# Performance work log

Measured on AMD Instinct MI355X. Metric: run time of the kernel, lower is better.

## Reference

```python
import jax, jax.numpy as jnp
from jax import lax
import numpy as np

LSTM = 128      # encoder hidden per direction
H2 = 2 * LSTM   # decoder hidden / bi-encoder output dim
E = 1024        # embedding dim
V = 30611       # vocab
A = 64          # attention dim
B, S, T = 16, 400, 96
START_TOK = 101


def setup_inputs() -> dict:
    key = jax.random.key(0)
    ks = jax.random.split(key, 24)
    d = {}
    d["word_embedding"] = jax.random.normal(ks[0], (V, E), jnp.float32) * 0.05
    d["article"] = jax.random.randint(ks[1], (B, S), 0, V)
    d["article_length"] = jax.random.randint(ks[2], (B,), S // 2, S + 1)
    d["abstract"] = jax.random.randint(ks[3], (B, T), 0, V)

    def p(k, shape, scale):
        return jax.random.normal(k, shape, jnp.float32) * scale

    # encoder BiLSTM (PyTorch gate order i,f,g,o), forward and backward dirs
    d["enc_Wih_f"] = p(ks[4], (4 * LSTM, E), 0.03)
    d["enc_Whh_f"] = p(ks[5], (4 * LSTM, LSTM), 0.08)
    d["enc_b_f"] = jnp.zeros((4 * LSTM,), jnp.float32)
    d["enc_Wih_b"] = p(ks[6], (4 * LSTM, E), 0.03)
    d["enc_Whh_b"] = p(ks[7], (4 * LSTM, LSTM), 0.08)
    d["enc_b_b"] = jnp.zeros((4 * LSTM,), jnp.float32)
    # decoder LSTM: input = embed(1024) + context(256)
    d["dec_Wih"] = p(ks[8], (4 * H2, E + H2), 0.03)
    d["dec_Whh"] = p(ks[9], (4 * H2, H2), 0.06)
    d["dec_b"] = jnp.zeros((4 * H2,), jnp.float32)
    # vocab prediction
    d["pred_W"] = p(ks[10], (V, H2), 0.06)
    d["pred_b"] = jnp.zeros((V,), jnp.float32)
    # additive attention
    d["attn_s_W"] = p(ks[11], (A, H2), 0.06)
    d["attn_s_b"] = jnp.zeros((A,), jnp.float32)
    d["attn_h_W"] = p(ks[12], (A, H2), 0.06)
    d["attn_h_b"] = jnp.zeros((A,), jnp.float32)
    d["attn_f_W"] = p(ks[13], (1, A), 0.12)
    d["attn_f_b"] = jnp.zeros((1,), jnp.float32)
    return d


def _lstm_cell(x, h, c, Wih, Whh, b):
    g = x @ Wih.T + h @ Whh.T + b
    i, f, gg, o = jnp.split(g, 4, axis=-1)
    c = jax.nn.sigmoid(f) * c + jax.nn.sigmoid(i) * jnp.tanh(gg)
    h = jax.nn.sigmoid(o) * jnp.tanh(c)
    return h, c


def reference(word_embedding, article, article_length, abstract,
              enc_Wih_f, enc_Whh_f, enc_b_f, enc_Wih_b, enc_Whh_b, enc_b_b,
              dec_Wih, dec_Whh, dec_b, pred_W, pred_b,
              attn_s_W, attn_s_b, attn_h_W, attn_h_b, attn_f_W, attn_f_b):
    dt = word_embedding.dtype
    # ---- encoder ----
    xe = word_embedding[article]          # [B,S,E]
    xs = xe.transpose(1, 0, 2)            # [S,B,E]
    z = jnp.zeros((B, LSTM), dt)

    def fstep(carry, x):
        h, c = carry
        h, c = _lstm_cell(x, h, c, enc_Wih_f, enc_Whh_f, enc_b_f)
        return (h, c), h

    def bstep(carry, x):
        h, c = carry
        h, c = _lstm_cell(x, h, c, enc_Wih_b, enc_Whh_b, enc_b_b)
        return (h, c), h

    (hf, cf_f), out_f = lax.scan(fstep, (z, z), xs)
    (hb, cf_b), out_b = lax.scan(bstep, (z, z), xs, reverse=True)
    enc_out = jnp.concatenate([out_f, out_b], axis=-1).transpose(1, 0, 2)  # [B,S,2H]

    # decoder init state = concat of final fwd/bwd encoder states
    h0 = jnp.concatenate([hf, hb], axis=-1)   # [B,H2]
    c0 = jnp.concatenate([cf_f, cf_b], axis=-1)

    # attention mask: (+9999 valid, -9999 pad); min(score, mask) keeps valid scores
    length = jnp.clip(article_length, 1, S)
    pos = jnp.arange(S)
    mask = jnp.where(pos[None, :] < length[:, None], 9999.0, -9999.0).astype(dt)

    enc_ws = enc_out @ attn_s_W.T + attn_s_b  # [B,S,A], precomputed per original code

    # teacher forcing inputs: step 0 uses token 101, step t uses abstract[:, t-1]
    tokens_in = jnp.concatenate(
        [jnp.full((B, 1), START_TOK, dtype=abstract.dtype), abstract[:, :-1]], axis=1)
    emb_in = word_embedding[tokens_in].transpose(1, 0, 2)  # [T,B,E]

    def dstep(carry, emb):
        h, c, ctx = carry
        x = jnp.concatenate([emb, ctx], axis=-1)           # [B,E+H2]
        h, c = _lstm_cell(x, h, c, dec_Wih, dec_Whh, dec_b)
        logits = h @ pred_W.T + pred_b                     # [B,V]
        wh = h @ attn_h_W.T + attn_h_b                     # [B,A]
        score = jnp.tanh(enc_ws + wh[:, None, :]) @ attn_f_W[0] + attn_f_b[0]  # [B,S]
        score = jnp.minimum(score, mask)
        w = jax.nn.softmax(score, axis=-1)
        ctx = jnp.einsum('bs,bsd->bd', w, enc_out)         # [B,H2]
        return (h, c, ctx), logits

    ctx0 = jnp.zeros((B, H2), dt)
    _, logits = lax.scan(dstep, (h0, c0, ctx0), emb_in)    # [T,B,V]

    logits = logits.transpose(1, 0, 2).reshape(B * T, V)
    tgt = abstract.reshape(-1)
    logp = jax.nn.log_softmax(logits, axis=-1)
    nll = -jnp.take_along_axis(logp, tgt[:, None], axis=1)[:, 0]
    valid = (tgt != 0).astype(logits.dtype)                # ignore_index=0
    loss = jnp.sum(nll * valid) / jnp.maximum(jnp.sum(valid), 1.0)
    return loss
```

## Files before the change

kernel.cpp:

```cpp
#include <hip/hip_runtime.h>
#include <cmath>

#define NB 16
#define SS 400
#define TT 96
#define HL 128
#define HH 256
#define AA 64
#define VV 30611
#define VVP 30720
#define START_TOK 101
#define NCHUNK 120

typedef __attribute__((ext_vector_type(8))) short bf16x8;
typedef __attribute__((ext_vector_type(4))) float f32x4;

#define PIN4(v) asm volatile("" : "+v"((v).x), "+v"((v).y), "+v"((v).z), "+v"((v).w))
#define LBAR() asm volatile("s_waitcnt lgkmcnt(0)\n\ts_barrier" ::: "memory")

__device__ __forceinline__ float gload(const float* p) {
  return __hip_atomic_load(p, __ATOMIC_RELAXED, __HIP_MEMORY_SCOPE_AGENT);
}
__device__ __forceinline__ void gstore(float* p, float v) {
  __hip_atomic_store(p, v, __ATOMIC_RELAXED, __HIP_MEMORY_SCOPE_AGENT);
}
__device__ __forceinline__ float sigmf(float x) { return 1.0f / (1.0f + __expf(-x)); }
__device__ __forceinline__ float tanhf_(float x) {
  float xc = fminf(fmaxf(x, -15.0f), 15.0f);
  return 1.0f - 2.0f / (__expf(2.0f * xc) + 1.0f);
}
__device__ __forceinline__ short f2bf(float f) {
  unsigned u = __float_as_uint(f);
  unsigned r = (u + 0x7FFFu + ((u >> 16) & 1u)) >> 16;
  return (short)r;
}
__device__ __forceinline__ void flagbar(int* flags, int b, int g, int target) {
  __syncthreads();
  if (threadIdx.x == 0)
    __hip_atomic_store(&flags[b*8 + g], target, __ATOMIC_RELAXED, __HIP_MEMORY_SCOPE_AGENT);
  if (threadIdx.x < 8) {
    while (__hip_atomic_load(&flags[b*8 + threadIdx.x], __ATOMIC_RELAXED, __HIP_MEMORY_SCOPE_AGENT) < target)
      __builtin_amdgcn_s_sleep(1);
  }
  LBAR();
}

__global__ __launch_bounds__(256) void k_init(int* flags) {
  if (threadIdx.x < 128) flags[threadIdx.x] = 0;
}

__global__ __launch_bounds__(256) void k_casts(
    const float* __restrict__ wf, const float* __restrict__ wb,
    const float* __restrict__ dwih,
    short* __restrict__ wfB, short* __restrict__ wbB, short* __restrict__ dwB)
{
  const int stride = gridDim.x * 256;
  const int t0 = blockIdx.x * 256 + threadIdx.x;
  for (int i = t0; i < 512*1024; i += stride) wfB[i] = f2bf(wf[i]);
  for (int i = t0; i < 512*1024; i += stride) wbB[i] = f2bf(wb[i]);
  for (int i = t0; i < 1024*1024; i += stride) {
    int r = i >> 10, k = i & 1023;
    dwB[i] = f2bf(dwih[r*1280 + k]);
  }
}

__global__ __launch_bounds__(256) void k_embproj_enc_mfma(
    const float* __restrict__ emb, const int* __restrict__ article,
    const short* __restrict__ wfB, const short* __restrict__ wbB,
    const float* __restrict__ bf, const float* __restrict__ bb,
    float* __restrict__ xcomb)
{
  const int m0 = blockIdx.x * 64;
  const int n0 = blockIdx.y * 256;
  const int t = threadIdx.x;
  const int w = t >> 6, l = t & 63;
  __shared__ short Abuf[64*136];
  __shared__ int tok[64];
  if (t < 64) {
    int R = m0 + t, s = R >> 4, b = R & 15;
    tok[t] = article[b*SS + s];
  }
  const short* __restrict__ Wb = (n0 < 512) ? wfB : wbB;
  const int nb0 = (n0 < 512) ? n0 : (n0 - 512);
  f32x4 acc[4][4];
  #pragma unroll
  for (int i = 0; i < 4; ++i)
    #pragma unroll
    for (int j = 0; j < 4; ++j) acc[i][j] = (f32x4){0.f,0.f,0.f,0.f};
  __syncthreads();
  const int ar = t >> 2, ak0 = (t & 3) * 32;
  for (int kc = 0; kc < 8; ++kc) {
    const float* src = emb + (size_t)tok[ar]*1024 + kc*128 + ak0;
    #pragma unroll
    for (int j = 0; j < 8; ++j) {
      float4 v = *(const float4*)(src + 4*j);
      short4 s4; s4.x = f2bf(v.x); s4.y = f2bf(v.y); s4.z = f2bf(v.z); s4.w = f2bf(v.w);
      *(short4*)(&Abuf[ar*136 + ak0 + 4*j]) = s4;
    }
    LBAR();
    #pragma unroll
    for (int ks = 0; ks < 4; ++ks) {
      bf16x8 af[4];
      #pragma unroll
      for (int mr = 0; mr < 4; ++mr)
        af[mr] = *(const bf16x8*)(&Abuf[(mr*16 + (l & 15))*136 + ks*32 + (l >> 4)*8]);
      #pragma unroll
      for (int ct = 0; ct < 4; ++ct) {
        int n = nb0 + w*64 + ct*16 + (l & 15);
        bf16x8 bfr = *(const bf16x8*)(Wb + (size_t)n*1024 + kc*128 + ks*32 + (l >> 4)*8);
        #pragma unroll
        for (int mr = 0; mr < 4; ++mr)
          acc[mr][ct] = __builtin_amdgcn_mfma_f32_16x16x32_bf16(af[mr], bfr, acc[mr][ct], 0, 0, 0);
      }
    }
    LBAR();
  }
  #pragma unroll
  for (int ct = 0; ct < 4; ++ct) {
    int n = n0 + w*64 + ct*16 + (l & 15);
    float bias = (n < 512) ? bf[n] : bb[n - 512];
    #pragma unroll
    for (int mr = 0; mr < 4; ++mr) {
      #pragma unroll
      for (int r = 0; r < 4; ++r) {
        int R = m0 + mr*16 + (l >> 4)*4 + r;
        xcomb[(size_t)R*1024 + n] = acc[mr][ct][r] + bias;
      }
    }
  }
}

__global__ __launch_bounds__(1024, 4) void k_encoder(
    const float* __restrict__ xcomb,
    const float* __restrict__ whhf, const float* __restrict__ whhb,
    float* __restrict__ encout,
    float* __restrict__ hpub,
    float* __restrict__ c0buf,
    const float* __restrict__ predW, short* __restrict__ predWb,
    const float* __restrict__ emb, const int* __restrict__ abstr,
    const short* __restrict__ dwB, const float* __restrict__ db,
    float* __restrict__ decpre)
{
  const int t = threadIdx.x;
  __shared__ float hl[128];
  __shared__ float part[2][512];
  __shared__ short Abuf[64*136];
  __shared__ int tok[64];

  if (blockIdx.x >= 56) {
    const size_t idx0 = (size_t)(blockIdx.x - 56) * 1024 + t;
    const size_t stride = (size_t)200 * 1024;
    for (size_t i = idx0; i < (size_t)VVP*256; i += stride)
      predWb[i] = (i < (size_t)VV*256) ? f2bf(predW[i]) : (short)0;
    return;
  }
  if (blockIdx.x >= 32) {
    const int m0 = (blockIdx.x - 32) * 64;
    const int sub = t & 255, w2 = t >> 8;
    const int w = sub >> 6, l = sub & 63;
    if (t < 64) {
      int R = m0 + t, tt2 = R >> 4, bb = R & 15;
      tok[t] = (tt2 == 0) ? START_TOK : abstr[bb*TT + tt2 - 1];
    }
    f32x4 acc[4][4];
    #pragma unroll
    for (int i = 0; i < 4; ++i)
      #pragma unroll
      for (int j = 0; j < 4; ++j) acc[i][j] = (f32x4){0.f,0.f,0.f,0.f};
    __syncthreads();
    const int ar = sub >> 2, ak0 = (sub & 3) * 32;
    for (int kc = 0; kc < 8; ++kc) {
      if (w2 == 0) {
        const float* src = emb + (size_t)tok[ar]*1024 + kc*128 + ak0;
        #pragma unroll
        for (int j = 0; j < 8; ++j) {
          float4 v = *(const float4*)(src + 4*j);
          short4 s4; s4.x = f2bf(v.x); s4.y = f2bf(v.y); s4.z = f2bf(v.z); s4.w = f2bf(v.w);
          *(short4*)(&Abuf[ar*136 + ak0 + 4*j]) = s4;
        }
      }
      LBAR();
      #pragma unroll
      for (int ks = 0; ks < 4; ++ks) {
        bf16x8 af[4];
        #pragma unroll
        for (int mr = 0; mr < 4; ++mr)
          af[mr] = *(const bf16x8*)(&Abuf[(mr*16 + (l & 15))*136 + ks*32 + (l >> 4)*8]);
        #pragma unroll
        for (int ct = 0; ct < 4; ++ct) {
          int n = w2*256 + w*64 + ct*16 + (l & 15);
          bf16x8 bfr = *(const bf16x8*)(dwB + (size_t)n*1024 + kc*128 + ks*32 + (l >> 4)*8);
          #pragma unroll
          for (int mr = 0; mr < 4; ++mr)
            acc[mr][ct] = __builtin_amdgcn_mfma_f32_16x16x32_bf16(af[mr], bfr, acc[mr][ct], 0, 0, 0);
        }
      }
      LBAR();
    }
    #pragma unroll
    for (int ct = 0; ct < 4; ++ct) {
      int n = w2*256 + w*64 + ct*16 + (l & 15);
      float bias = db[n];
      #pragma unroll
      for (int mr = 0; mr < 4; ++mr) {
        #pragma unroll
        for (int r = 0; r < 4; ++r) {
          int R = m0 + mr*16 + (l >> 4)*4 + r;
          decpre[(size_t)R*1024 + n] = acc[mr][ct][r] + bias;
        }
      }
    }
    return;
  }
  const int b = blockIdx.x & 15, dir = blockIdx.x >> 4;
  const int row = t & 511;
  const int ks = t >> 9;
  const float* __restrict__ Whh = dir ? whhb : whhf;
  float4 wr[16];
  #pragma unroll
  for (int j = 0; j < 16; ++j) {
    wr[j] = *(const float4*)(Whh + row*128 + ks*64 + j*4);
    PIN4(wr[j]);
  }
  float c_reg = 0.0f;
  if (t < 128) hl[t] = 0.0f;
  float xv0 = 0.f, xv1 = 0.f, xv2 = 0.f, xv3 = 0.f;
  if (t < 128) {
    const float* xr = xcomb + ((dir ? (SS-1) : 0)*NB + b)*1024 + dir*512 + t;
    xv0 = xr[0]; xv1 = xr[128]; xv2 = xr[256]; xv3 = xr[384];
  }
  __syncthreads();
  for (int s = 0; s < SS; ++s) {
    const int sf = dir ? (SS-1-s) : s;
    const float* hs = hl + ks*64;
    float a0 = 0.f, a1 = 0.f, a2 = 0.f, a3 = 0.f;
    #pragma unroll
    for (int j = 0; j < 16; j += 4) {
      float4 h0 = *(const float4*)(hs + j*4);
      float4 h1 = *(const float4*)(hs + j*4 + 4);
      float4 h2 = *(const float4*)(hs + j*4 + 8);
      float4 h3 = *(const float4*)(hs + j*4 + 12);
      a0 += wr[j].x*h0.x + wr[j].y*h0.y + wr[j].z*h0.z + wr[j].w*h0.w;
      a1 += wr[j+1].x*h1.x + wr[j+1].y*h1.y + wr[j+1].z*h1.z + wr[j+1].w*h1.w;
      a2 += wr[j+2].x*h2.x + wr[j+2].y*h2.y + wr[j+2].z*h2.z + wr[j+2].w*h2.w;
      a3 += wr[j+3].x*h3.x + wr[j+3].y*h3.y + wr[j+3].z*h3.z + wr[j+3].w*h3.w;
    }
    part[ks][row] = (a0 + a1) + (a2 + a3);
    float nx0 = 0.f, nx1 = 0.f, nx2 = 0.f, nx3 = 0.f;
    if (t < 128 && s + 1 < SS) {
      const int sfn = dir ? (SS-2-s) : (s+1);
      const float* xr = xcomb + (sfn*NB + b)*1024 + dir*512 + t;
      nx0 = xr[0]; nx1 = xr[128]; nx2 = xr[256]; nx3 = xr[384];
    }
    LBAR();
    if (t < 128) {
      float gi = part[0][t]       + part[1][t]       + xv0;
      float gf = part[0][128 + t] + part[1][128 + t] + xv1;
      float gg = part[0][256 + t] + part[1][256 + t] + xv2;
      float go = part[0][384 + t] + part[1][384 + t] + xv3;
      float iv = sigmf(gi), fv = sigmf(gf), gv = tanhf_(gg), ov = sigmf(go);
      c_reg = fv*c_reg + iv*gv;
      float hv = ov*tanhf_(c_reg);
      hl[t] = hv;
      encout[(b*SS + sf)*HH + dir*HL + t] = hv;
    }
    LBAR();
    xv0 = nx0; xv1 = nx1; xv2 = nx2; xv3 = nx3;
  }
  if (t < 128) {
    hpub[b*HH + dir*HL + t] = hl[t];
    c0buf[b*HH + dir*HL + t] = c_reg;
  }
}

__global__ __launch_bounds__(256) void k_encws(
    const float* __restrict__ encout,
    const float* __restrict__ asW, const float* __restrict__ asb,
    float* __restrict__ encwsR)
{
  const int rt = blockIdx.x;
  const int tid = threadIdx.x;
  __shared__ float Al[32*260];
  #pragma unroll
  for (int i = 0; i < 32; ++i) {
    int l = tid + i*256;
    int r = l >> 8, k = l & 255;
    Al[r*260 + k] = encout[(rt*32 + r)*256 + k];
  }
  __syncthreads();
  const int a = tid & 63, rg = tid >> 6;
  float acc[8];
  #pragma unroll
  for (int q = 0; q < 8; ++q) acc[q] = 0.0f;
  const float4* w4 = (const float4*)(asW + a*256);
  for (int k4 = 0; k4 < 64; ++k4) {
    float4 w = w4[k4];
    #pragma unroll
    for (int q = 0; q < 8; ++q) {
      const float4* a4 = (const float4*)(Al + (rg*8 + q)*260);
      float4 av = a4[k4];
      acc[q] += av.x*w.x + av.y*w.y + av.z*w.z + av.w*w.w;
    }
  }
  float bias = asb[a];
  #pragma unroll
  for (int q = 0; q < 8; ++q) {
    int row = rt*32 + rg*8 + q;
    encwsR[row*64 + a] = acc[q] + bias;
  }
}

__global__ __launch_bounds__(1024, 4) void k_decoder(
    const float* __restrict__ decpre,
    const float* __restrict__ dwhh,
    const float* __restrict__ dwih,
    const float* __restrict__ ahW, const float* __restrict__ ahb,
    const float* __restrict__ afW, const float* __restrict__ afb,
    const float* __restrict__ encwsR,
    const float* __restrict__ encout,
    const int* __restrict__ alen,
    const float* __restrict__ c0buf,
    float* hpub, float* cpub, float* wpub,
    float* __restrict__ dhall,
    int* flags)
{
  const int wg = blockIdx.x;
  const int g = wg >> 4, b = wg & 15;
  const int t = threadIdx.x;
  const int r = t & 127, ks = t >> 7;
  const int lane = t & 63;
  const int u = t & 31;
  const int s0 = g*50;

  const int grow = (r >> 5)*256 + g*32 + (r & 31);
  float4 wr[16];
  #pragma unroll
  for (int j = 0; j < 16; ++j) {
    int k = ks*64 + j*4;
    wr[j] = (k < 256) ? *(const float4*)(dwhh + grow*256 + k)
                      : *(const float4*)(dwih + grow*1280 + 1024 + (k - 256));
    PIN4(wr[j]);
  }

  __shared__ float encl[50*256];
  __shared__ float wsl[50*68];
  __shared__ float ahWt[32*68];
  __shared__ float hc[512];
  __shared__ float part[8][132];
  __shared__ float wh[64];
  __shared__ float fwl[64];
  __shared__ float scl[64];
  __shared__ float sh_m, sh_s;

  for (int i = t; i < 50*256; i += 1024) {
    int si = i >> 8, d = i & 255;
    encl[i] = encout[(b*SS + s0 + si)*HH + d];
  }
  for (int i = t; i < 50*64; i += 1024) {
    int si = i >> 6, a = i & 63;
    wsl[si*68 + a] = encwsR[(b*SS + s0 + si)*64 + a];
  }
  for (int i = t; i < 32*64; i += 1024) {
    int u2 = i >> 6, a = i & 63;
    ahWt[u2*68 + a] = ahW[a*HH + g*32 + u2];
  }
  if (t < 64) fwl[t] = afW[t];
  const float fb0 = afb[0];
  int len = alen[b]; len = min(max(len, 1), SS);
  float c_reg = 0.f;
  float pre0 = 0.f, pre1 = 0.f, pre2 = 0.f, pre3 = 0.f;
  if (t < 256) {
    c_reg = c0buf[b*HH + g*32 + u];
    hc[t] = gload(hpub + b*HH + t);
    hc[256 + t] = 0.0f;
    const float* pr = decpre + (size_t)(0*NB + b)*1024 + g*32 + u;
    pre0 = pr[0]; pre1 = pr[256]; pre2 = pr[512]; pre3 = pr[768];
  }
  __syncthreads();

  for (int tt = 0; tt < TT; ++tt) {
    {
      const float* hs = hc + ks*64;
      float a0 = 0.f, a1 = 0.f, a2 = 0.f, a3 = 0.f;
      #pragma unroll
      for (int j = 0; j < 16; j += 4) {
        float4 h0 = *(const float4*)(hs + j*4);
        float4 h1 = *(const float4*)(hs + j*4 + 4);
        float4 h2 = *(const float4*)(hs + j*4 + 8);
        float4 h3 = *(const float4*)(hs + j*4 + 12);
        a0 += wr[j].x*h0.x + wr[j].y*h0.y + wr[j].z*h0.z + wr[j].w*h0.w;
        a1 += wr[j+1].x*h1.x + wr[j+1].y*h1.y + wr[j+1].z*h1.z + wr[j+1].w*h1.w;
        a2 += wr[j+2].x*h2.x + wr[j+2].y*h2.y + wr[j+2].z*h2.z + wr[j+2].w*h2.w;
        a3 += wr[j+3].x*h3.x + wr[j+3].y*h3.y + wr[j+3].z*h3.z + wr[j+3].w*h3.w;
      }
      part[ks][r] = (a0 + a1) + (a2 + a3);
    }
    LBAR();
    if (t < 256) {
      float g0 = pre0, g1 = pre1, g2 = pre2, g3 = pre3;
      #pragma unroll
      for (int j = 0; j < 8; ++j) {
        g0 += part[j][u];
        g1 += part[j][32 + u];
        g2 += part[j][64 + u];
        g3 += part[j][96 + u];
      }
      float iv = sigmf(g0), fv = sigmf(g1), gv = tanhf_(g2), ov = sigmf(g3);
      c_reg = fv*c_reg + iv*gv;
      float hv = ov*tanhf_(c_reg);
      if (t < 32) {
        gstore(hpub + b*HH + g*32 + t, hv);
        dhall[(tt*NB + b)*HH + g*32 + t] = hv;
      }
      int wv = t >> 6;
      int a = wv*16 + (lane >> 2);
      int j4 = lane & 3;
      float wacc = 0.f;
      #pragma unroll
      for (int i = 0; i < 8; ++i) {
        int u2 = j4*8 + i;
        float hx = __shfl(hv, u2, 64);
        wacc += ahWt[u2*68 + a] * hx;
      }
      wacc += __shfl_xor(wacc, 1);
      wacc += __shfl_xor(wacc, 2);
      if (j4 == 0) gstore(wpub + (b*8 + g)*72 + a, wacc);
    }
    flagbar(flags, b, g, 2*tt + 1);
    if (t < 256) {
      hc[t] = gload(hpub + b*HH + t);
      if (tt + 1 < TT) {
        const float* pr = decpre + (size_t)((tt+1)*NB + b)*1024 + g*32 + u;
        pre0 = pr[0]; pre1 = pr[256]; pre2 = pr[512]; pre3 = pr[768];
      }
    } else if (t < 320) {
      int a = t - 256;
      float s = ahb[a];
      #pragma unroll
      for (int j = 0; j < 8; ++j) s += gload(wpub + (b*8 + j)*72 + a);
      wh[a] = s;
    }
    LBAR();
    if (t < 800) {
      int s = t >> 4, j = t & 15;
      const float* wrow = wsl + s*68 + j*4;
      float p = fwl[j*4]   * tanhf_(wrow[0] + wh[j*4])
              + fwl[j*4+1] * tanhf_(wrow[1] + wh[j*4+1])
              + fwl[j*4+2] * tanhf_(wrow[2] + wh[j*4+2])
              + fwl[j*4+3] * tanhf_(wrow[3] + wh[j*4+3]);
      p += __shfl_xor(p, 1);
      p += __shfl_xor(p, 2);
      p += __shfl_xor(p, 4);
      p += __shfl_xor(p, 8);
      if (j == 0) scl[s] = p;
    }
    LBAR();
    if (t < 64) {
      float sc = -1e30f;
      if (t < 50) {
        sc = fb0 + scl[t];
        sc = fminf(sc, (s0 + t < len) ? 9999.0f : -9999.0f);
      }
      float m = sc;
      #pragma unroll
      for (int o = 32; o; o >>= 1) m = fmaxf(m, __shfl_xor(m, o));
      float p = (t < 50) ? __expf(sc - m) : 0.0f;
      scl[t] = p;
      float ssum = p;
      #pragma unroll
      for (int o = 32; o; o >>= 1) ssum += __shfl_xor(ssum, o);
      if (t == 0) { sh_m = m; sh_s = ssum; }
    }
    LBAR();
    if (t < 256) {
      float acc = 0.0f;
      const float* eb = encl + t;
      #pragma unroll 10
      for (int i = 0; i < 50; ++i) acc += scl[i] * eb[i*256];
      gstore(cpub + (b*8 + g)*272 + t, acc);
      if (t == 0) gstore(cpub + (b*8 + g)*272 + 256, sh_m);
      if (t == 1) gstore(cpub + (b*8 + g)*272 + 257, sh_s);
    }
    flagbar(flags, b, g, 2*tt + 2);
    if (t < 256) {
      float mj[8], sj[8];
      #pragma unroll
      for (int j = 0; j < 8; ++j) {
        mj[j] = gload(cpub + (b*8 + j)*272 + 256);
        sj[j] = gload(cpub + (b*8 + j)*272 + 257);
      }
      float M = mj[0];
      #pragma unroll
      for (int j = 1; j < 8; ++j) M = fmaxf(M, mj[j]);
      float denom = 0.f, ctx = 0.f;
      #pragma unroll
      for (int j = 0; j < 8; ++j) {
        float e = __expf(mj[j] - M);
        denom += sj[j] * e;
        ctx += gload(cpub + (b*8 + j)*272 + t) * e;
      }
      hc[256 + t] = ctx / denom;
    }
    LBAR();
  }
}

__global__ __launch_bounds__(256) void k_pred_mfma(
    const float* __restrict__ dhall,
    const short* __restrict__ predWb,
    const float* __restrict__ predb,
    float* __restrict__ pm, float* __restrict__ ps)
{
  const int m0 = blockIdx.x * 64;
  const int ch = blockIdx.y;
  const int c0 = ch * 256;
  const int t = threadIdx.x;
  const int w = t >> 6, l = t & 63;
  __shared__ __align__(16) char smem[64*264*4];
  short* Abuf = (short*)smem;
  float* L    = (float*)smem;
  __shared__ float red[256];
  __shared__ float rowmax[64];

  {
    const int ar = t >> 2, ak0 = (t & 3) * 64;
    const float* src = dhall + (size_t)(m0 + ar)*256 + ak0;
    #pragma unroll
    for (int j = 0; j < 16; ++j) {
      float4 v = *(const float4*)(src + 4*j);
      short4 s4; s4.x = f2bf(v.x); s4.y = f2bf(v.y); s4.z = f2bf(v.z); s4.w = f2bf(v.w);
      *(short4*)(&Abuf[ar*264 + ak0 + 4*j]) = s4;
    }
  }
  LBAR();
  f32x4 acc[4][4];
  #pragma unroll
  for (int i = 0; i < 4; ++i)
    #pragma unroll
    for (int j = 0; j < 4; ++j) acc[i][j] = (f32x4){0.f,0.f,0.f,0.f};
  #pragma unroll
  for (int kst = 0; kst < 8; ++kst) {
    bf16x8 af[4];
    #pragma unroll
    for (int mr = 0; mr < 4; ++mr)
      af[mr] = *(const bf16x8*)(&Abuf[(mr*16 + (l & 15))*264 + kst*32 + (l >> 4)*8]);
    #pragma unroll
    for (int ct = 0; ct < 4; ++ct) {
      int col = c0 + w*64 + ct*16 + (l & 15);
      bf16x8 bfr = *(const bf16x8*)(predWb + (size_t)col*256 + kst*32 + (l >> 4)*8);
      #pragma unroll
      for (int mr = 0; mr < 4; ++mr)
        acc[mr][ct] = __builtin_amdgcn_mfma_f32_16x16x32_bf16(af[mr], bfr, acc[mr][ct], 0, 0, 0);
    }
  }
  LBAR();
  #pragma unroll
  for (int ct = 0; ct < 4; ++ct) {
    int col = c0 + w*64 + ct*16 + (l & 15);
    float bias = (col < VV) ? predb[col] : 0.0f;
    bool valid = (col < VV);
    #pragma unroll
    for (int mr = 0; mr < 4; ++mr) {
      #pragma unroll
      for (int r = 0; r < 4; ++r) {
        int rl = mr*16 + (l >> 4)*4 + r;
        L[rl*264 + w*64 + ct*16 + (l & 15)] = valid ? (acc[mr][ct][r] + bias) : -1e30f;
      }
    }
  }
  LBAR();
  {
    const int row = t & 63, qd = t >> 6;
    float m = -1e30f;
    const float* Lr = L + row*264 + qd*64;
    for (int i = 0; i < 64; ++i) m = fmaxf(m, Lr[i]);
    red[qd*64 + row] = m;
  }
  LBAR();
  if (t < 64) {
    float m = fmaxf(fmaxf(red[t], red[64+t]), fmaxf(red[128+t], red[192+t]));
    rowmax[t] = m;
  }
  LBAR();
  {
    const int row = t & 63, qd = t >> 6;
    float m = rowmax[row];
    float ssum = 0.f;
    const float* Lr = L + row*264 + qd*64;
    for (int i = 0; i < 64; ++i) ssum += __expf(Lr[i] - m);
    red[qd*64 + row] = ssum;
  }
  LBAR();
  if (t < 64) {
    float ssum = red[t] + red[64+t] + red[128+t] + red[192+t];
    pm[(m0 + t)*NCHUNK + ch] = rowmax[t];
    ps[(m0 + t)*NCHUNK + ch] = ssum;
  }
}

__global__ __launch_bounds__(256) void k_loss_part(
    const float* __restrict__ pm, const float* __restrict__ ps,
    const float* __restrict__ dhall,
    const float* __restrict__ predW, const float* __restrict__ predb,
    const int* __restrict__ abstr, float* __restrict__ lpart)
{
  const int tid = threadIdx.x;
  const int row = blockIdx.x*256 + tid;
  __shared__ float rs[256], rc[256];
  float lsum = 0.0f, lcnt = 0.0f;
  {
    int t = row >> 4, b = row & 15;
    int tok = abstr[b*TT + t];
    float m = -1e30f;
    for (int c = 0; c < NCHUNK; ++c) m = fmaxf(m, pm[row*NCHUNK + c]);
    float ss = 0.0f;
    for (int c = 0; c < NCHUNK; ++c) ss += ps[row*NCHUNK + c] * __expf(pm[row*NCHUNK + c] - m);
    float lse = m + __logf(ss);
    float tl = predb[tok];
    const float* hrow = dhall + row*256;
    const float* wrow = predW + tok*256;
    #pragma unroll 4
    for (int k = 0; k < 256; ++k) tl += hrow[k] * wrow[k];
    if (tok != 0) { lsum = lse - tl; lcnt = 1.0f; }
  }
  rs[tid] = lsum; rc[tid] = lcnt;
  __syncthreads();
  for (int st = 128; st; st >>= 1) {
    if (tid < st) { rs[tid] += rs[tid + st]; rc[tid] += rc[tid + st]; }
    __syncthreads();
  }
  if (tid == 0) { lpart[blockIdx.x*2] = rs[0]; lpart[blockIdx.x*2 + 1] = rc[0]; }
}

__global__ void k_loss_final(const float* __restrict__ lpart, float* __restrict__ out) {
  if (threadIdx.x == 0) {
    float s = 0.f, c = 0.f;
    for (int i = 0; i < 6; ++i) { s += lpart[i*2]; c += lpart[i*2 + 1]; }
    out[0] = s / fmaxf(c, 1.0f);
  }
}

extern "C" void kernel_launch(void* const* d_in, const int* in_sizes, int n_in,
                              void* d_out, int out_size, void* d_ws, size_t ws_size,
                              hipStream_t stream) {
  const float* emb   = (const float*)d_in[0];
  const int* article = (const int*)d_in[1];
  const int* alen    = (const int*)d_in[2];
  const int* abstr   = (const int*)d_in[3];
  const float* eWihF = (const float*)d_in[4];
  const float* eWhhF = (const float*)d_in[5];
  const float* ebF   = (const float*)d_in[6];
  const float* eWihB = (const float*)d_in[7];
  const float* eWhhB = (const float*)d_in[8];
  const float* ebB   = (const float*)d_in[9];
  const float* dWih  = (const float*)d_in[10];
  const float* dWhh  = (const float*)d_in[11];
  const float* db    = (const float*)d_in[12];
  const float* pW    = (const float*)d_in[13];
  const float* pb    = (const float*)d_in[14];
  const float* asW   = (const float*)d_in[15];
  const float* asb   = (const float*)d_in[16];
  const float* ahW   = (const float*)d_in[17];
  const float* ahb   = (const float*)d_in[18];
  const float* afW   = (const float*)d_in[19];
  const float* afb   = (const float*)d_in[20];
  float* out = (float*)d_out;

  float* w = (float*)d_ws;
  size_t o = 0;
  float* xcomb  = w + o; o += (size_t)SS*NB*1024;
  float* encout = w + o; o += (size_t)NB*SS*HH;
  float* encwsR = w + o; o += (size_t)NB*SS*AA;
  float* decpre = w + o; o += (size_t)TT*NB*1024;
  float* dhall  = w + o; o += (size_t)TT*NB*HH;
  float* hpub   = w + o; o += NB*HH;
  float* cpub   = w + o; o += NB*8*272;
  float* wpub   = w + o; o += NB*8*72;
  float* c0buf  = w + o; o += NB*HH;
  float* pm     = w + o; o += (size_t)TT*NB*NCHUNK;
  float* ps     = w + o; o += (size_t)TT*NB*NCHUNK;
  float* lpart  = w + o; o += 16;
  int* flags = (int*)(w + o); o += 128;
  short* predWb = (short*)(w + o); o += (size_t)VVP*256/2;
  short* wfB    = (short*)(w + o); o += 512*1024/2;
  short* wbB    = (short*)(w + o); o += 512*1024/2;
  short* dwB    = (short*)(w + o); o += 1024*1024/2;

  k_init<<<1, 256, 0, stream>>>(flags);
  k_casts<<<512, 256, 0, stream>>>(eWihF, eWihB, dWih, wfB, wbB, dwB);
  k_embproj_enc_mfma<<<dim3(100, 4), 256, 0, stream>>>(emb, article, wfB, wbB, ebF, ebB, xcomb);
  k_encoder<<<256, 1024, 0, stream>>>(xcomb, eWhhF, eWhhB, encout, hpub, c0buf,
                                      pW, predWb, emb, abstr, dwB, db, decpre);
  k_encws<<<200, 256, 0, stream>>>(encout, asW, asb, encwsR);
  k_decoder<<<128, 1024, 0, stream>>>(decpre, dWhh, dWih, ahW, ahb, afW, afb,
                                      encwsR, encout, alen, c0buf, hpub, cpub, wpub, dhall, flags);
  k_pred_mfma<<<dim3(24, 120), 256, 0, stream>>>(dhall, predWb, pb, pm, ps);
  k_loss_part<<<6, 256, 0, stream>>>(pm, ps, dhall, pW, pb, abstr, lpart);
  k_loss_final<<<1, 64, 0, stream>>>(lpart, out);
}
```

Before: 1.604 ms.

## Fuse decoder and vocab projection into one persistent kernel with progress flags

Merges the decoder recurrence, the encoder attention projection (previously a separate k_encws kernel) and the vocab-prediction GEMM into one launch of 256 workgroups. The first 128 workgroups run the recurrent decoder and publish per-batch progress counters. The other 128 poll those counters and compute logits plus per-chunk softmax statistics for completed timestep groups while decoding continues. This overlaps the large vocab GEMM with the latency-bound serial decoder and removes two launches. The risks are that the spin-waiting workgroups must be co-resident with the decoder workgroups to avoid deadlock, and that the prediction workgroups now use 1024 threads with smaller per-wave tiles.

After: 1.809 ms. +12.8%, slower.

```diff
diff --git a/kernel.cpp b/kernel.cpp
--- a/kernel.cpp
+++ b/kernel.cpp
@@ -21,6 +21,9 @@
 __device__ __forceinline__ float gload(const float* p) {
   return __hip_atomic_load(p, __ATOMIC_RELAXED, __HIP_MEMORY_SCOPE_AGENT);
 }
+__device__ __forceinline__ int gload_i(const int* p) {
+  return __hip_atomic_load(p, __ATOMIC_RELAXED, __HIP_MEMORY_SCOPE_AGENT);
+}
 __device__ __forceinline__ void gstore(float* p, float v) {
   __hip_atomic_store(p, v, __ATOMIC_RELAXED, __HIP_MEMORY_SCOPE_AGENT);
 }
@@ -46,7 +49,7 @@
 }
 
 __global__ __launch_bounds__(256) void k_init(int* flags) {
-  if (threadIdx.x < 128) flags[threadIdx.x] = 0;
+  if (threadIdx.x < 160) flags[threadIdx.x] = 0;
 }
 
 __global__ __launch_bounds__(256) void k_casts(
@@ -273,328 +276,306 @@
   }
 }
 
-__global__ __launch_bounds__(256) void k_encws(
-    const float* __restrict__ encout,
-    const float* __restrict__ asW, const float* __restrict__ asb,
-    float* __restrict__ encwsR)
-{
-  const int rt = blockIdx.x;
-  const int tid = threadIdx.x;
-  __shared__ float Al[32*260];
-  #pragma unroll
-  for (int i = 0; i < 32; ++i) {
-    int l = tid + i*256;
-    int r = l >> 8, k = l & 255;
-    Al[r*260 + k] = encout[(rt*32 + r)*256 + k];
-  }
-  __syncthreads();
-  const int a = tid & 63, rg = tid >> 6;
-  float acc[8];
-  #pragma unroll
-  for (int q = 0; q < 8; ++q) acc[q] = 0.0f;
-  const float4* w4 = (const float4*)(asW + a*256);
-  for (int k4 = 0; k4 < 64; ++k4) {
-    float4 w = w4[k4];
-    #pragma unroll
-    for (int q = 0; q < 8; ++q) {
-      const float4* a4 = (const float4*)(Al + (rg*8 + q)*260);
-      float4 av = a4[k4];
-      acc[q] += av.x*w.x + av.y*w.y + av.z*w.z + av.w*w.w;
-    }
-  }
-  float bias = asb[a];
-  #pragma unroll
-  for (int q = 0; q < 8; ++q) {
-    int row = rt*32 + rg*8 + q;
-    encwsR[row*64 + a] = acc[q] + bias;
-  }
-}
-
-__global__ __launch_bounds__(1024, 4) void k_decoder(
+__global__ __launch_bounds__(1024, 4) void k_decoder_pred(
     const float* __restrict__ decpre,
     const float* __restrict__ dwhh,
     const float* __restrict__ dwih,
     const float* __restrict__ ahW, const float* __restrict__ ahb,
     const float* __restrict__ afW, const float* __restrict__ afb,
-    const float* __restrict__ encwsR,
+    const float* __restrict__ asW, const float* __restrict__ asb,
     const float* __restrict__ encout,
     const int* __restrict__ alen,
     const float* __restrict__ c0buf,
     float* hpub, float* cpub, float* wpub,
     float* __restrict__ dhall,
-    int* flags)
-{
-  const int wg = blockIdx.x;
-  const int g = wg >> 4, b = wg & 15;
-  const int t = threadIdx.x;
-  const int r = t & 127, ks = t >> 7;
-  const int lane = t & 63;
-  const int u = t & 31;
-  const int s0 = g*50;
-
-  const int grow = (r >> 5)*256 + g*32 + (r & 31);
-  float4 wr[16];
-  #pragma unroll
-  for (int j = 0; j < 16; ++j) {
-    int k = ks*64 + j*4;
-    wr[j] = (k < 256) ? *(const float4*)(dwhh + grow*256 + k)
-                      : *(const float4*)(dwih + grow*1280 + 1024 + (k - 256));
-    PIN4(wr[j]);
-  }
-
-  __shared__ float encl[50*256];
-  __shared__ float wsl[50*68];
-  __shared__ float ahWt[32*68];
-  __shared__ float hc[512];
-  __shared__ float part[8][132];
-  __shared__ float wh[64];
-  __shared__ float fwl[64];
-  __shared__ float scl[64];
-  __shared__ float sh_m, sh_s;
-
-  for (int i = t; i < 50*256; i += 1024) {
-    int si = i >> 8, d = i & 255;
-    encl[i] = encout[(b*SS + s0 + si)*HH + d];
-  }
-  for (int i = t; i < 50*64; i += 1024) {
-    int si = i >> 6, a = i & 63;
-    wsl[si*68 + a] = encwsR[(b*SS + s0 + si)*64 + a];
-  }
-  for (int i = t; i < 32*64; i += 1024) {
-    int u2 = i >> 6, a = i & 63;
-    ahWt[u2*68 + a] = ahW[a*HH + g*32 + u2];
-  }
-  if (t < 64) fwl[t] = afW[t];
-  const float fb0 = afb[0];
-  int len = alen[b]; len = min(max(len, 1), SS);
-  float c_reg = 0.f;
-  float pre0 = 0.f, pre1 = 0.f, pre2 = 0.f, pre3 = 0.f;
-  if (t < 256) {
-    c_reg = c0buf[b*HH + g*32 + u];
-    hc[t] = gload(hpub + b*HH + t);
-    hc[256 + t] = 0.0f;
-    const float* pr = decpre + (size_t)(0*NB + b)*1024 + g*32 + u;
-    pre0 = pr[0]; pre1 = pr[256]; pre2 = pr[512]; pre3 = pr[768];
-  }
-  __syncthreads();
-
-  for (int tt = 0; tt < TT; ++tt) {
-    {
-      const float* hs = hc + ks*64;
-      float a0 = 0.f, a1 = 0.f, a2 = 0.f, a3 = 0.f;
-      #pragma unroll
-      for (int j = 0; j < 16; j += 4) {
-        float4 h0 = *(const float4*)(hs + j*4);
-        float4 h1 = *(const float4*)(hs + j*4 + 4);
-        float4 h2 = *(const float4*)(hs + j*4 + 8);
-        float4 h3 = *(const float4*)(hs + j*4 + 12);
-        a0 += wr[j].x*h0.x + wr[j].y*h0.y + wr[j].z*h0.z + wr[j].w*h0.w;
-        a1 += wr[j+1].x*h1.x + wr[j+1].y*h1.y + wr[j+1].z*h1.z + wr[j+1].w*h1.w;
-        a2 += wr[j+2].x*h2.x + wr[j+2].y*h2.y + wr[j+2].z*h2.z + wr[j+2].w*h2.w;
-        a3 += wr[j+3].x*h3.x + wr[j+3].y*h3.y + wr[j+3].z*h3.z + wr[j+3].w*h3.w;
-      }
-      part[ks][r] = (a0 + a1) + (a2 + a3);
-    }
-    LBAR();
-    if (t < 256) {
-      float g0 = pre0, g1 = pre1, g2 = pre2, g3 = pre3;
-      #pragma unroll
-      for (int j = 0; j < 8; ++j) {
-        g0 += part[j][u];
-        g1 += part[j][32 + u];
-        g2 += part[j][64 + u];
-        g3 += part[j][96 + u];
-      }
-      float iv = sigmf(g0), fv = sigmf(g1), gv = tanhf_(g2), ov = sigmf(g3);
-      c_reg = fv*c_reg + iv*gv;
-      float hv = ov*tanhf_(c_reg);
-      if (t < 32) {
-        gstore(hpub + b*HH + g*32 + t, hv);
-        dhall[(tt*NB + b)*HH + g*32 + t] = hv;
-      }
-      int wv = t >> 6;
-      int a = wv*16 + (lane >> 2);
-      int j4 = lane & 3;
-      float wacc = 0.f;
-      #pragma unroll
-      for (int i = 0; i < 8; ++i) {
-        int u2 = j4*8 + i;
-        float hx = __shfl(hv, u2, 64);
-        wacc += ahWt[u2*68 + a] * hx;
-      }
-      wacc += __shfl_xor(wacc, 1);
-      wacc += __shfl_xor(wacc, 2);
-      if (j4 == 0) gstore(wpub + (b*8 + g)*72 + a, wacc);
-    }
-    flagbar(flags, b, g, 2*tt + 1);
-    if (t < 256) {
-      hc[t] = gload(hpub + b*HH + t);
-      if (tt + 1 < TT) {
-        const float* pr = decpre + (size_t)((tt+1)*NB + b)*1024 + g*32 + u;
-        pre0 = pr[0]; pre1 = pr[256]; pre2 = pr[512]; pre3 = pr[768];
-      }
-    } else if (t < 320) {
-      int a = t - 256;
-      float s = ahb[a];
-      #pragma unroll
-      for (int j = 0; j < 8; ++j) s += gload(wpub + (b*8 + j)*72 + a);
-      wh[a] = s;
-    }
-    LBAR();
-    if (t < 800) {
-      int s = t >> 4, j = t & 15;
-      const float* wrow = wsl + s*68 + j*4;
-      float p = fwl[j*4]   * tanhf_(wrow[0] + wh[j*4])
-              + fwl[j*4+1] * tanhf_(wrow[1] + wh[j*4+1])
-              + fwl[j*4+2] * tanhf_(wrow[2] + wh[j*4+2])
-              + fwl[j*4+3] * tanhf_(wrow[3] + wh[j*4+3]);
-      p += __shfl_xor(p, 1);
-      p += __shfl_xor(p, 2);
-      p += __shfl_xor(p, 4);
-      p += __shfl_xor(p, 8);
-      if (j == 0) scl[s] = p;
-    }
-    LBAR();
-    if (t < 64) {
-      float sc = -1e30f;
-      if (t < 50) {
-        sc = fb0 + scl[t];
-        sc = fminf(sc, (s0 + t < len) ? 9999.0f : -9999.0f);
-      }
-      float m = sc;
-      #pragma unroll
-      for (int o = 32; o; o >>= 1) m = fmaxf(m, __shfl_xor(m, o));
-      float p = (t < 50) ? __expf(sc - m) : 0.0f;
-      scl[t] = p;
-      float ssum = p;
-      #pragma unroll
-      for (int o = 32; o; o >>= 1) ssum += __shfl_xor(ssum, o);
-      if (t == 0) { sh_m = m; sh_s = ssum; }
-    }
-    LBAR();
-    if (t < 256) {
-      float acc = 0.0f;
-      const float* eb = encl + t;
-      #pragma unroll 10
-      for (int i = 0; i < 50; ++i) acc += scl[i] * eb[i*256];
-      gstore(cpub + (b*8 + g)*272 + t, acc);
-      if (t == 0) gstore(cpub + (b*8 + g)*272 + 256, sh_m);
-      if (t == 1) gstore(cpub + (b*8 + g)*272 + 257, sh_s);
-    }
-    flagbar(flags, b, g, 2*tt + 2);
-    if (t < 256) {
-      float mj[8], sj[8];
-      #pragma unroll
-      for (int j = 0; j < 8; ++j) {
-        mj[j] = gload(cpub + (b*8 + j)*272 + 256);
-        sj[j] = gload(cpub + (b*8 + j)*272 + 257);
-      }
-      float M = mj[0];
-      #pragma unroll
-      for (int j = 1; j < 8; ++j) M = fmaxf(M, mj[j]);
-      float denom = 0.f, ctx = 0.f;
-      #pragma unroll
-      for (int j = 0; j < 8; ++j) {
-        float e = __expf(mj[j] - M);
-        denom += sj[j] * e;
-        ctx += gload(cpub + (b*8 + j)*272 + t) * e;
-      }
-      hc[256 + t] = ctx / denom;
-    }
-    LBAR();
-  }
-}
-
-__global__ __launch_bounds__(256) void k_pred_mfma(
-    const float* __restrict__ dhall,
+    int* flags,
     const short* __restrict__ predWb,
     const float* __restrict__ predb,
     float* __restrict__ pm, float* __restrict__ ps)
 {
-  const int m0 = blockIdx.x * 64;
-  const int ch = blockIdx.y;
-  const int c0 = ch * 256;
+  __shared__ __align__(16) float smem[20140];
+  int* prog = flags + 128;
   const int t = threadIdx.x;
-  const int w = t >> 6, l = t & 63;
-  __shared__ __align__(16) char smem[64*264*4];
-  short* Abuf = (short*)smem;
-  float* L    = (float*)smem;
-  __shared__ float red[256];
-  __shared__ float rowmax[64];
-
-  {
-    const int ar = t >> 2, ak0 = (t & 3) * 64;
-    const float* src = dhall + (size_t)(m0 + ar)*256 + ak0;
+
+  if (blockIdx.x < 128) {
+    float* encl = smem;
+    float* wsl  = smem + 12800;
+    float* ahWt = smem + 16200;
+    float* hc   = smem + 18376;
+    float* part = smem + 18888;
+    float* wh   = smem + 19944;
+    float* fwl  = smem + 20008;
+    float* scl  = smem + 20072;
+    float* shms = smem + 20136;
+
+    const int wg = blockIdx.x;
+    const int g = wg >> 4, b = wg & 15;
+    const int r = t & 127, ks = t >> 7;
+    const int lane = t & 63;
+    const int u = t & 31;
+    const int s0 = g*50;
+    const int grow = (r >> 5)*256 + g*32 + (r & 31);
+    float4 wr[16];
     #pragma unroll
     for (int j = 0; j < 16; ++j) {
-      float4 v = *(const float4*)(src + 4*j);
-      short4 s4; s4.x = f2bf(v.x); s4.y = f2bf(v.y); s4.z = f2bf(v.z); s4.w = f2bf(v.w);
-      *(short4*)(&Abuf[ar*264 + ak0 + 4*j]) = s4;
-    }
-  }
-  LBAR();
-  f32x4 acc[4][4];
-  #pragma unroll
-  for (int i = 0; i < 4; ++i)
-    #pragma unroll
-    for (int j = 0; j < 4; ++j) acc[i][j] = (f32x4){0.f,0.f,0.f,0.f};
-  #pragma unroll
-  for (int kst = 0; kst < 8; ++kst) {
-    bf16x8 af[4];
-    #pragma unroll
-    for (int mr = 0; mr < 4; ++mr)
-      af[mr] = *(const bf16x8*)(&Abuf[(mr*16 + (l & 15))*264 + kst*32 + (l >> 4)*8]);
-    #pragma unroll
-    for (int ct = 0; ct < 4; ++ct) {
-      int col = c0 + w*64 + ct*16 + (l & 15);
-      bf16x8 bfr = *(const bf16x8*)(predWb + (size_t)col*256 + kst*32 + (l >> 4)*8);
-      #pragma unroll
-      for (int mr = 0; mr < 4; ++mr)
-        acc[mr][ct] = __builtin_amdgcn_mfma_f32_16x16x32_bf16(af[mr], bfr, acc[mr][ct], 0, 0, 0);
-    }
-  }
-  LBAR();
-  #pragma unroll
-  for (int ct = 0; ct < 4; ++ct) {
-    int col = c0 + w*64 + ct*16 + (l & 15);
-    float bias = (col < VV) ? predb[col] : 0.0f;
-    bool valid = (col < VV);
-    #pragma unroll
-    for (int mr = 0; mr < 4; ++mr) {
-      #pragma unroll
-      for (int r = 0; r < 4; ++r) {
-        int rl = mr*16 + (l >> 4)*4 + r;
-        L[rl*264 + w*64 + ct*16 + (l & 15)] = valid ? (acc[mr][ct][r] + bias) : -1e30f;
-      }
-    }
-  }
-  LBAR();
-  {
-    const int row = t & 63, qd = t >> 6;
-    float m = -1e30f;
-    const float* Lr = L + row*264 + qd*64;
-    for (int i = 0; i < 64; ++i) m = fmaxf(m, Lr[i]);
-    red[qd*64 + row] = m;
-  }
-  LBAR();
-  if (t < 64) {
-    float m = fmaxf(fmaxf(red[t], red[64+t]), fmaxf(red[128+t], red[192+t]));
-    rowmax[t] = m;
-  }
-  LBAR();
-  {
-    const int row = t & 63, qd = t >> 6;
-    float m = rowmax[row];
-    float ssum = 0.f;
-    const float* Lr = L + row*264 + qd*64;
-    for (int i = 0; i < 64; ++i) ssum += __expf(Lr[i] - m);
-    red[qd*64 + row] = ssum;
-  }
-  LBAR();
-  if (t < 64) {
-    float ssum = red[t] + red[64+t] + red[128+t] + red[192+t];
-    pm[(m0 + t)*NCHUNK + ch] = rowmax[t];
-    ps[(m0 + t)*NCHUNK + ch] = ssum;
+      int k = ks*64 + j*4;
+      wr[j] = (k < 256) ? *(const float4*)(dwhh + grow*256 + k)
+                        : *(const float4*)(dwih + grow*1280 + 1024 + (k - 256));
+      PIN4(wr[j]);
+    }
+    for (int i = t; i < 50*256; i += 1024) {
+      int si = i >> 8, d = i & 255;
+      encl[i] = encout[(b*SS + s0 + si)*HH + d];
+    }
+    for (int i = t; i < 32*64; i += 1024) {
+      int u2 = i >> 6, a = i & 63;
+      ahWt[u2*68 + a] = ahW[a*HH + g*32 + u2];
+    }
+    if (t < 64) fwl[t] = afW[t];
+    LBAR();
+    {
+      const int a = t & 63;
+      const float4* w4 = (const float4*)(asW + a*256);
+      for (int si = t >> 6; si < 50; si += 16) {
+        const float4* er4 = (const float4*)(encl + si*256);
+        float acc = 0.f;
+        #pragma unroll 8
+        for (int k4 = 0; k4 < 64; ++k4) {
+          float4 wv = w4[k4]; float4 ev = er4[k4];
+          acc += wv.x*ev.x + wv.y*ev.y + wv.z*ev.z + wv.w*ev.w;
+        }
+        wsl[si*68 + a] = acc + asb[a];
+      }
+    }
+    const float fb0 = afb[0];
+    int len = alen[b]; len = min(max(len, 1), SS);
+    float c_reg = 0.f;
+    float pre0 = 0.f, pre1 = 0.f, pre2 = 0.f, pre3 = 0.f;
+    if (t < 256) {
+      c_reg = c0buf[b*HH + g*32 + u];
+      hc[t] = gload(hpub + b*HH + t);
+      hc[256 + t] = 0.0f;
+      const float* pr = decpre + (size_t)(0*NB + b)*1024 + g*32 + u;
+      pre0 = pr[0]; pre1 = pr[256]; pre2 = pr[512]; pre3 = pr[768];
+    }
+    __syncthreads();
+
+    for (int tt = 0; tt < TT; ++tt) {
+      {
+        const float* hs = hc + ks*64;
+        float a0 = 0.f, a1 = 0.f, a2 = 0.f, a3 = 0.f;
+        #pragma unroll
+        for (int j = 0; j < 16; j += 4) {
+          float4 h0 = *(const float4*)(hs + j*4);
+          float4 h1 = *(const float4*)(hs + j*4 + 4);
+          float4 h2 = *(const float4*)(hs + j*4 + 8);
+          float4 h3 = *(const float4*)(hs + j*4 + 12);
+          a0 += wr[j].x*h0.x + wr[j].y*h0.y + wr[j].z*h0.z + wr[j].w*h0.w;
+          a1 += wr[j+1].x*h1.x + wr[j+1].y*h1.y + wr[j+1].z*h1.z + wr[j+1].w*h1.w;
+          a2 += wr[j+2].x*h2.x + wr[j+2].y*h2.y + wr[j+2].z*h2.z + wr[j+2].w*h2.w;
+          a3 += wr[j+3].x*h3.x + wr[j+3].y*h3.y + wr[j+3].z*h3.z + wr[j+3].w*h3.w;
+        }
+        part[ks*132 + r] = (a0 + a1) + (a2 + a3);
+      }
+      LBAR();
+      if (t < 256) {
+        float g0 = pre0, g1 = pre1, g2 = pre2, g3 = pre3;
+        #pragma unroll
+        for (int j = 0; j < 8; ++j) {
+          g0 += part[j*132 + u];
+          g1 += part[j*132 + 32 + u];
+          g2 += part[j*132 + 64 + u];
+          g3 += part[j*132 + 96 + u];
+        }
+        float iv = sigmf(g0), fv = sigmf(g1), gv = tanhf_(g2), ov = sigmf(g3);
+        c_reg = fv*c_reg + iv*gv;
+        float hv = ov*tanhf_(c_reg);
+        if (t < 32) {
+          gstore(hpub + b*HH + g*32 + t, hv);
+          gstore(dhall + (size_t)(tt*NB + b)*HH + g*32 + t, hv);
+        }
+        int wv = t >> 6;
+        int a = wv*16 + (lane >> 2);
+        int j4 = lane & 3;
+        float wacc = 0.f;
+        #pragma unroll
+        for (int i = 0; i < 8; ++i) {
+          int u2 = j4*8 + i;
+          float hx = __shfl(hv, u2, 64);
+          wacc += ahWt[u2*68 + a] * hx;
+        }
+        wacc += __shfl_xor(wacc, 1);
+        wacc += __shfl_xor(wacc, 2);
+        if (j4 == 0) gstore(wpub + (b*8 + g)*72 + a, wacc);
+      }
+      flagbar(flags, b, g, 2*tt + 1);
+      if (g == 0 && t == 0)
+        __hip_atomic_store(&prog[b], tt + 1, __ATOMIC_RELAXED, __HIP_MEMORY_SCOPE_AGENT);
+      if (t < 256) {
+        hc[t] = gload(hpub + b*HH + t);
+        if (tt + 1 < TT) {
+          const float* pr = decpre + (size_t)((tt+1)*NB + b)*1024 + g*32 + u;
+          pre0 = pr[0]; pre1 = pr[256]; pre2 = pr[512]; pre3 = pr[768];
+        }
+      } else if (t < 320) {
+        int a = t - 256;
+        float s = ahb[a];
+        #pragma unroll
+        for (int j = 0; j < 8; ++j) s += gload(wpub + (b*8 + j)*72 + a);
+        wh[a] = s;
+      }
+      LBAR();
+      if (t < 800) {
+        int s = t >> 4, j = t & 15;
+        const float* wrow = wsl + s*68 + j*4;
+        float p = fwl[j*4]   * tanhf_(wrow[0] + wh[j*4])
+                + fwl[j*4+1] * tanhf_(wrow[1] + wh[j*4+1])
+                + fwl[j*4+2] * tanhf_(wrow[2] + wh[j*4+2])
+                + fwl[j*4+3] * tanhf_(wrow[3] + wh[j*4+3]);
+        p += __shfl_xor(p, 1);
+        p += __shfl_xor(p, 2);
+        p += __shfl_xor(p, 4);
+        p += __shfl_xor(p, 8);
+        if (j == 0) scl[s] = p;
+      }
+      LBAR();
+      if (t < 64) {
+        float sc = -1e30f;
+        if (t < 50) {
+          sc = fb0 + scl[t];
+          sc = fminf(sc, (s0 + t < len) ? 9999.0f : -9999.0f);
+        }
+        float m = sc;
+        #pragma unroll
+        for (int o = 32; o; o >>= 1) m = fmaxf(m, __shfl_xor(m, o));
+        float p = (t < 50) ? __expf(sc - m) : 0.0f;
+        scl[t] = p;
+        float ssum = p;
+        #pragma unroll
+        for (int o = 32; o; o >>= 1) ssum += __shfl_xor(ssum, o);
+        if (t == 0) { shms[0] = m; shms[1] = ssum; }
+      }
+      LBAR();
+      if (t < 256) {
+        float acc = 0.0f;
+        const float* eb = encl + t;
+        #pragma unroll 10
+        for (int i = 0; i < 50; ++i) acc += scl[i] * eb[i*256];
+        gstore(cpub + (b*8 + g)*272 + t, acc);
+        if (t == 0) gstore(cpub + (b*8 + g)*272 + 256, shms[0]);
+        if (t == 1) gstore(cpub + (b*8 + g)*272 + 257, shms[1]);
+      }
+      flagbar(flags, b, g, 2*tt + 2);
+      if (t < 256) {
+        float mj[8], sj[8];
+        #pragma unroll
+        for (int j = 0; j < 8; ++j) {
+          mj[j] = gload(cpub + (b*8 + j)*272 + 256);
+          sj[j] = gload(cpub + (b*8 + j)*272 + 257);
+        }
+        float M = mj[0];
+        #pragma unroll
+        for (int j = 1; j < 8; ++j) M = fmaxf(M, mj[j]);
+        float denom = 0.f, ctx = 0.f;
+        #pragma unroll
+        for (int j = 0; j < 8; ++j) {
+          float e = __expf(mj[j] - M);
+          denom += sj[j] * e;
+          ctx += gload(cpub + (b*8 + j)*272 + t) * e;
+        }
+        hc[256 + t] = ctx / denom;
+      }
+      LBAR();
+    }
+  } else {
+    short* Abuf = (short*)smem;
+    float* L    = smem;
+    float* red  = smem + 16896;
+    float* rowmax = smem + 17920;
+    const int hw = blockIdx.x - 128;
+    const int w = t >> 6, l = t & 63;
+
+    for (int k = 0; k < 23; ++k) {
+      int item = hw + 128*k;
+      if (item >= 24*120) break;
+      int tt4 = item / 120, ch = item - tt4*120;
+      int m0 = tt4*64, c0 = ch*256;
+      int target = 4*tt4 + 4;
+      if (t < 16)
+        while (gload_i(prog + t) < target) __builtin_amdgcn_s_sleep(64);
+      __syncthreads();
+      #pragma unroll
+      for (int j = 0; j < 16; ++j) {
+        int e = t + j*1024;
+        int row = e >> 8, col = e & 255;
+        Abuf[row*264 + col] = f2bf(gload(dhall + (size_t)(m0 + row)*256 + col));
+      }
+      LBAR();
+      f32x4 acc[4];
+      #pragma unroll
+      for (int i = 0; i < 4; ++i) acc[i] = (f32x4){0.f,0.f,0.f,0.f};
+      #pragma unroll
+      for (int kst = 0; kst < 8; ++kst) {
+        bf16x8 af[4];
+        #pragma unroll
+        for (int mr = 0; mr < 4; ++mr)
+          af[mr] = *(const bf16x8*)(&Abuf[(mr*16 + (l & 15))*264 + kst*32 + (l >> 4)*8]);
+        int col = c0 + w*16 + (l & 15);
+        bf16x8 bfr = *(const bf16x8*)(predWb + (size_t)col*256 + kst*32 + (l >> 4)*8);
+        #pragma unroll
+        for (int mr = 0; mr < 4; ++mr)
+          acc[mr] = __builtin_amdgcn_mfma_f32_16x16x32_bf16(af[mr], bfr, acc[mr], 0, 0, 0);
+      }
+      LBAR();
+      {
+        int col = c0 + w*16 + (l & 15);
+        float bias = (col < VV) ? predb[col] : 0.0f;
+        bool valid = (col < VV);
+        #pragma unroll
+        for (int mr = 0; mr < 4; ++mr) {
+          #pragma unroll
+          for (int rr = 0; rr < 4; ++rr) {
+            int rl = mr*16 + (l >> 4)*4 + rr;
+            L[rl*264 + w*16 + (l & 15)] = valid ? (acc[mr][rr] + bias) : -1e30f;
+          }
+        }
+      }
+      LBAR();
+      {
+        const int row = t & 63, qd = t >> 6;
+        float m = -1e30f;
+        const float* Lr = L + row*264 + qd*16;
+        #pragma unroll
+        for (int i = 0; i < 16; ++i) m = fmaxf(m, Lr[i]);
+        red[qd*64 + row] = m;
+      }
+      LBAR();
+      if (t < 64) {
+        float m = -1e30f;
+        #pragma unroll
+        for (int qd = 0; qd < 16; ++qd) m = fmaxf(m, red[qd*64 + t]);
+        rowmax[t] = m;
+      }
+      LBAR();
+      {
+        const int row = t & 63, qd = t >> 6;
+        float m = rowmax[row];
+        float ssum = 0.f;
+        const float* Lr = L + row*264 + qd*16;
+        #pragma unroll
+        for (int i = 0; i < 16; ++i) ssum += __expf(Lr[i] - m);
+        red[qd*64 + row] = ssum;
+      }
+      LBAR();
+      if (t < 64) {
+        float ssum = 0.f;
+        #pragma unroll
+        for (int qd = 0; qd < 16; ++qd) ssum += red[qd*64 + t];
+        pm[(m0 + t)*NCHUNK + ch] = rowmax[t];
+        ps[(m0 + t)*NCHUNK + ch] = ssum;
+      }
+      LBAR();
+    }
   }
 }
 
@@ -670,7 +651,6 @@
   size_t o = 0;
   float* xcomb  = w + o; o += (size_t)SS*NB*1024;
   float* encout = w + o; o += (size_t)NB*SS*HH;
-  float* encwsR = w + o; o += (size_t)NB*SS*AA;
   float* decpre = w + o; o += (size_t)TT*NB*1024;
   float* dhall  = w + o; o += (size_t)TT*NB*HH;
   float* hpub   = w + o; o += NB*HH;
@@ -680,7 +660,7 @@
   float* pm     = w + o; o += (size_t)TT*NB*NCHUNK;
   float* ps     = w + o; o += (size_t)TT*NB*NCHUNK;
   float* lpart  = w + o; o += 16;
-  int* flags = (int*)(w + o); o += 128;
+  int* flags = (int*)(w + o); o += 256;
   short* predWb = (short*)(w + o); o += (size_t)VVP*256/2;
   short* wfB    = (short*)(w + o); o += 512*1024/2;
   short* wbB    = (short*)(w + o); o += 512*1024/2;
@@ -691,10 +671,10 @@
   k_embproj_enc_mfma<<<dim3(100, 4), 256, 0, stream>>>(emb, article, wfB, wbB, ebF, ebB, xcomb);
   k_encoder<<<256, 1024, 0, stream>>>(xcomb, eWhhF, eWhhB, encout, hpub, c0buf,
                                       pW, predWb, emb, abstr, dwB, db, decpre);
-  k_encws<<<200, 256, 0, stream>>>(encout, asW, asb, encwsR);
-  k_decoder<<<128, 1024, 0, stream>>>(decpre, dWhh, dWih, ahW, ahb, afW, afb,
-                                      encwsR, encout, alen, c0buf, hpub, cpub, wpub, dhall, flags);
-  k_pred_mfma<<<dim3(24, 120), 256, 0, stream>>>(dhall, predWb, pb, pm, ps);
+  k_decoder_pred<<<256, 1024, 0, stream>>>(decpre, dWhh, dWih, ahW, ahb, afW, afb,
+                                           asW, asb, encout, alen, c0buf,
+                                           hpub, cpub, wpub, dhall, flags,
+                                           predWb, pb, pm, ps);
   k_loss_part<<<6, 256, 0, stream>>>(pm, ps, dhall, pW, pb, abstr, lpart);
   k_loss_final<<<1, 64, 0, stream>>>(lpart, out);
 }
```
